# Performance work log

Hardware: AMD Instinct MI355X
Metric: run time of the kernel (lower is better)

Reference implementation:

```python
import jax, jax.numpy as jnp
import numpy as np


def setup_inputs() -> dict:
    key = jax.random.key(0)
    ks = jax.random.split(key, 5)
    B = 8192
    return {
        "x": jax.random.normal(ks[0], (B, 1, 28, 28), dtype=jnp.float32),
        "conv1w": jax.random.normal(ks[1], (3, 196, 1, 2, 2), dtype=jnp.float32),
        "conv2w": jax.random.normal(ks[2], (64, 36, 3, 4, 4), dtype=jnp.float32),
        "fc1w": jax.random.normal(ks[3], (1024, 2304), dtype=jnp.float32),
        "fc2w": jax.random.normal(ks[4], (10, 1024), dtype=jnp.float32),
    }


def reference(x, conv1w, conv2w, fc1w, fc2w):
    # The torch module swaps a fresh filter into conv2d for every output pixel,
    # i.e. an unshared-weight (locally-connected) conv. Each kept pixel is
    # relu(dot(patch, per-pixel filter)), so we unfold patches and contract.
    B = x.shape[0]

    # --- layer 1: 2x2 kernel, stride 2, non-overlapping -> 14x14 = 196 pixels
    # [B,1,28,28] -> [B,14,2,14,2] -> [B,196,4] patches
    p1 = x[:, 0].reshape(B, 14, 2, 14, 2).transpose(0, 1, 3, 2, 4).reshape(B, 196, 4)
    w1 = conv1w.reshape(3, 196, 4)  # [C=3, P=196, K=4]
    out1 = jax.nn.relu(jnp.einsum('bpk,cpk->bcp', p1, w1)).reshape(B, 3, 14, 14)

    # --- layer 2: 4x4 kernel, stride 2 on 14x14 -> 6x6 = 36 pixels, 3 in-ch
    idx = 2 * jnp.arange(6)[:, None] + jnp.arange(4)[None, :]  # [6,4] row/col gather
    t = out1[:, :, idx, :]          # [B,3,6,4,14]
    t = t[:, :, :, :, idx]          # [B,3,6,4,6,4]
    # -> [B, 6, 6, 3, 4, 4] -> [B, 36, 48] (patch features in torch CHW order)
    p2 = t.transpose(0, 2, 4, 1, 3, 5).reshape(B, 36, 48)
    w2 = conv2w.reshape(64, 36, 48)  # [C=64, P=36, K=48]
    out2 = jax.nn.relu(jnp.einsum('bpk,cpk->bcp', p2, w2)).reshape(B, 2304)

    # --- fully connected head (bias-free linears)
    h = jax.nn.relu(out2 @ fc1w.T)   # [B,1024]
    return h @ fc2w.T                # [B,10]
```

## Files before the change

kernel.cpp:

```cpp
#include <hip/hip_runtime.h>
#include <hip/hip_bf16.h>

typedef __attribute__((ext_vector_type(8))) short short8;
typedef __attribute__((ext_vector_type(4))) float f32x4;
typedef __attribute__((ext_vector_type(8))) unsigned short ushort8;
typedef __attribute__((ext_vector_type(4))) unsigned short ushort4v;

__device__ __forceinline__ float bf2f(unsigned short u) {
  union { unsigned int i; float f; } v;
  v.i = ((unsigned int)u) << 16;
  return v.f;
}

__device__ __forceinline__ unsigned short f2bf(float f) {
  union { float f; unsigned int i; } v;
  v.f = f;
  unsigned int x = v.i;
  return (unsigned short)((x + 0x7FFFu + ((x >> 16) & 1u)) >> 16);
}

__device__ __forceinline__ void async_load16(const void* g, void* l) {
  __builtin_amdgcn_global_load_lds(
      (const __attribute__((address_space(1))) unsigned int*)g,
      (__attribute__((address_space(3))) unsigned int*)l, 16, 0, 0);
}

__global__ __launch_bounds__(256) void cvt_permute(
    const float* __restrict__ fc1, unsigned short* __restrict__ out) {
  __shared__ float row[2304];
  const int n = blockIdx.x;
  const float* src = fc1 + (size_t)n * 2304;
  for (int i = threadIdx.x; i < 2304; i += 256) row[i] = src[i];
  __syncthreads();
  unsigned short* dst = out + (size_t)n * 2304;
  for (int i = threadIdx.x; i < 2304; i += 256) {
    int pp = i >> 6, c2 = i & 63;
    dst[i] = f2bf(row[c2 * 36 + pp]);
  }
}

#define LDP 72
__global__ __launch_bounds__(256) void conv_fused3(
    const float* __restrict__ x, const float* __restrict__ w1,
    const float* __restrict__ w2, unsigned short* __restrict__ out2, int B) {
  __shared__ unsigned short s_w2[64 * LDP];
  __shared__ unsigned short s_win[64 * LDP];
  const int tid = threadIdx.x;
  const int b0 = blockIdx.x * 64;
  const int p = blockIdx.y;
  const int u = p / 6, u2 = p % 6;

  {
    const float* w2p = w2 + (size_t)p * 48;
    for (int it = tid; it < 768; it += 256) {
      int c2 = it & 63, q = it >> 6;
      float4 wv = *(const float4*)(w2p + (size_t)c2 * 1728 + 4 * q);
      ushort4v o;
      o[0] = f2bf(wv.x); o[1] = f2bf(wv.y); o[2] = f2bf(wv.z); o[3] = f2bf(wv.w);
      *(ushort4v*)&s_w2[c2 * LDP + 4 * q] = o;
    }
  }

  for (int it = tid; it < 768; it += 256) {
    int bi = it & 63, cv = it >> 6;
    int c = cv >> 2, v = cv & 3;
    int pi = 2 * u + v;
    const float* xb = x + (size_t)(b0 + bi) * 784 + pi * 56 + 4 * u2;
    float4 a0 = *(const float4*)xb;
    float4 a1 = *(const float4*)(xb + 4);
    float4 r0 = *(const float4*)(xb + 28);
    float4 r1 = *(const float4*)(xb + 32);
    const float* wbase = w1 + ((c * 196 + pi * 14 + 2 * u2) << 2);
    float4 q0 = *(const float4*)(wbase);
    float4 q1 = *(const float4*)(wbase + 4);
    float4 q2 = *(const float4*)(wbase + 8);
    float4 q3 = *(const float4*)(wbase + 12);
    ushort4v o;
    o[0] = f2bf(fmaxf(a0.x * q0.x + a0.y * q0.y + r0.x * q0.z + r0.y * q0.w, 0.f));
    o[1] = f2bf(fmaxf(a0.z * q1.x + a0.w * q1.y + r0.z * q1.z + r0.w * q1.w, 0.f));
    o[2] = f2bf(fmaxf(a1.x * q2.x + a1.y * q2.y + r1.x * q2.z + r1.y * q2.w, 0.f));
    o[3] = f2bf(fmaxf(a1.z * q3.x + a1.w * q3.y + r1.z * q3.z + r1.w * q3.w, 0.f));
    *(ushort4v*)&s_win[bi * LDP + 4 * cv] = o;
  }

  {
    int bi = tid >> 2, q = tid & 3;
    ushort4v z = {0, 0, 0, 0};
    *(ushort4v*)&s_win[bi * LDP + 48 + 4 * q] = z;
    *(ushort4v*)&s_w2[bi * LDP + 48 + 4 * q] = z;
  }
  __syncthreads();

  const int lane = tid & 63, wave = tid >> 6;
  const int wm = wave >> 1, wn = wave & 1;
  const int fr = lane & 15, fo = (lane >> 4) * 8;
  f32x4 acc[2][2] = {};
  #pragma unroll
  for (int k2 = 0; k2 < 2; ++k2) {
    short8 af[2], bf[2];
    #pragma unroll
    for (int m = 0; m < 2; ++m)
      af[m] = *(const short8*)&s_win[(wm * 32 + m * 16 + fr) * LDP + k2 * 32 + fo];
    #pragma unroll
    for (int n = 0; n < 2; ++n)
      bf[n] = *(const short8*)&s_w2[(wn * 32 + n * 16 + fr) * LDP + k2 * 32 + fo];
    #pragma unroll
    for (int m = 0; m < 2; ++m)
      #pragma unroll
      for (int n = 0; n < 2; ++n)
        acc[m][n] =
            __builtin_amdgcn_mfma_f32_16x16x32_bf16(af[m], bf[n], acc[m][n], 0, 0, 0);
  }
  __syncthreads();

  unsigned short* s_out = s_win;
  const int r0 = wm * 32 + (lane >> 4) * 4;
  const int c0 = wn * 32 + fr;
  #pragma unroll
  for (int m = 0; m < 2; ++m)
    #pragma unroll
    for (int n = 0; n < 2; ++n)
      #pragma unroll
      for (int j = 0; j < 4; ++j)
        s_out[(r0 + m * 16 + j) * 64 + (c0 + n * 16)] =
            f2bf(fmaxf(acc[m][n][j], 0.f));
  __syncthreads();

  for (int it = tid; it < 512; it += 256) {
    int row = it >> 3, ch = it & 7;
    *(short8*)(out2 + (size_t)(b0 + row) * 2304 + p * 64 + ch * 8) =
        *(const short8*)&s_out[row * 64 + ch * 8];
  }
}

#define GBM 128
#define GBN 128
#define GBK 64

__global__ __launch_bounds__(512) void gemm_fc1_fc2(
    const unsigned short* __restrict__ A,
    const unsigned short* __restrict__ Bw,
    const float* __restrict__ Wfc2,
    float* __restrict__ out,
    int K, int NT) {
  __shared__ unsigned short sA[2 * GBM * GBK];
  __shared__ unsigned short sB[2 * GBN * GBK];
  __shared__ float sW[10 * GBN];
  const int tid = threadIdx.x;
  const int lane = tid & 63;
  const int wave = tid >> 6;
  const int wm = wave >> 2, wn = wave & 3;
  const size_t m0 = (size_t)blockIdx.x * GBM;
  const size_t n0 = (size_t)blockIdx.y * GBN;

  const int r8 = tid >> 3;
  const int c8 = tid & 7;
  const int ksw = (c8 ^ (r8 & 7)) * 8;
  const unsigned short* Ag = A + (m0 + r8) * (size_t)K + ksw;
  const unsigned short* Bg = Bw + (n0 + r8) * (size_t)K + ksw;
  unsigned short* sAp = &sA[r8 * GBK + c8 * 8];
  unsigned short* sBp = &sB[r8 * GBK + c8 * 8];

#define STAGE_A(buf, t, i) \
  async_load16(Ag + (size_t)(t) * GBK + (size_t)(i) * 64 * K, \
               sAp + (buf) * (GBM * GBK) + (i) * 64 * GBK)
#define STAGE_B(buf, t, i) \
  async_load16(Bg + (size_t)(t) * GBK + (size_t)(i) * 64 * K, \
               sBp + (buf) * (GBN * GBK) + (i) * 64 * GBK)
#define STAGE_TILE(buf, t) \
  STAGE_A(buf, t, 0); STAGE_A(buf, t, 1); STAGE_B(buf, t, 0); STAGE_B(buf, t, 1)

  STAGE_TILE(0, 0);

  const int fr = lane & 15, fg = lane >> 4, fx = lane & 7;
  int aBase[4], bBase[2];
  #pragma unroll
  for (int m = 0; m < 4; ++m) aBase[m] = (wm * 64 + m * 16 + fr) * GBK;
  #pragma unroll
  for (int n = 0; n < 2; ++n) bBase[n] = (wn * 32 + n * 16 + fr) * GBK;
  const int jc0 = (fg ^ fx) * 8;
  const int jc1 = jc0 ^ 32;

  f32x4 acc[4][2] = {};

  for (int t = 0; t < NT; ++t) {
    const int cur = t & 1;
    if (t + 1 < NT) {
      STAGE_TILE(cur ^ 1, t + 1);
      asm volatile("s_waitcnt vmcnt(4)" ::: "memory");
    } else {
      asm volatile("s_waitcnt vmcnt(0)" ::: "memory");
    }
    __builtin_amdgcn_s_barrier();

    const unsigned short* As = &sA[cur * GBM * GBK];
    const unsigned short* Bs = &sB[cur * GBN * GBK];
    short8 a0[4], a1[4], b0[2], b1[2];
    #pragma unroll
    for (int m = 0; m < 4; ++m) {
      a0[m] = *(const short8*)&As[aBase[m] + jc0];
      a1[m] = *(const short8*)&As[aBase[m] + jc1];
    }
    #pragma unroll
    for (int n = 0; n < 2; ++n) {
      b0[n] = *(const short8*)&Bs[bBase[n] + jc0];
      b1[n] = *(const short8*)&Bs[bBase[n] + jc1];
    }
    __builtin_amdgcn_s_setprio(1);
    #pragma unroll
    for (int m = 0; m < 4; ++m)
      #pragma unroll
      for (int n = 0; n < 2; ++n)
        acc[m][n] = __builtin_amdgcn_mfma_f32_16x16x32_bf16(a0[m], b0[n],
                                                            acc[m][n], 0, 0, 0);
    #pragma unroll
    for (int m = 0; m < 4; ++m)
      #pragma unroll
      for (int n = 0; n < 2; ++n)
        acc[m][n] = __builtin_amdgcn_mfma_f32_16x16x32_bf16(a1[m], b1[n],
                                                            acc[m][n], 0, 0, 0);
    __builtin_amdgcn_s_setprio(0);
    __builtin_amdgcn_s_barrier();
  }

  for (int i = tid; i < 10 * GBN; i += 512)
    sW[i] = Wfc2[(i >> 7) * 1024 + n0 + (i & 127)];

  unsigned short* hs = sA;
  #pragma unroll
  for (int m = 0; m < 4; ++m)
    #pragma unroll
    for (int n = 0; n < 2; ++n)
      #pragma unroll
      for (int j = 0; j < 4; ++j) {
        int row = wm * 64 + m * 16 + fg * 4 + j;
        int col = wn * 32 + n * 16 + fr;
        hs[row * 128 + (col ^ ((row & 7) << 3))] =
            f2bf(fmaxf(acc[m][n][j], 0.f));
      }
  __syncthreads();

  {
    const int row = tid >> 2;
    const int quar = tid & 3;
    const int r7s = (row & 7) << 3;
    float hv[32];
    #pragma unroll
    for (int c = 0; c < 4; ++c) {
      int base = quar * 32 + c * 8;
      short8 u = *(const short8*)&hs[row * 128 + (base ^ r7s)];
      #pragma unroll
      for (int q = 0; q < 8; ++q) hv[c * 8 + q] = bf2f((unsigned short)u[q]);
    }
    float* op = out + (m0 + row) * 10;
    #pragma unroll
    for (int o = 0; o < 10; ++o) {
      const float* wr = &sW[o * 128 + quar * 32];
      float a = 0.f;
      #pragma unroll
      for (int q = 0; q < 32; ++q) a += hv[q] * wr[q];
      a += __shfl_down(a, 1);
      a += __shfl_down(a, 2);
      if (quar == 0) atomicAdd(&op[o], a);
    }
  }
#undef STAGE_A
#undef STAGE_B
#undef STAGE_TILE
}

extern "C" void kernel_launch(void* const* d_in, const int* in_sizes, int n_in,
                              void* d_out, int out_size, void* d_ws, size_t ws_size,
                              hipStream_t stream) {
  const float* x   = (const float*)d_in[0];
  const float* w1  = (const float*)d_in[1];
  const float* w2  = (const float*)d_in[2];
  const float* fc1 = (const float*)d_in[3];
  const float* fc2 = (const float*)d_in[4];
  float* out = (float*)d_out;
  const int B = in_sizes[0] / 784;

  unsigned short* out2 = (unsigned short*)d_ws;
  unsigned short* fc1b = out2 + (size_t)B * 2304;

  hipMemsetAsync(out, 0, (size_t)out_size * sizeof(float), stream);
  cvt_permute<<<1024, 256, 0, stream>>>(fc1, fc1b);
  dim3 cg(B / 64, 36);
  conv_fused3<<<cg, 256, 0, stream>>>(x, w1, w2, out2, B);
  dim3 g(B / GBM, 1024 / GBN);
  gemm_fc1_fc2<<<g, 512, 0, stream>>>(out2, fc1b, fc2, out, 2304, 2304 / GBK);
}
```

Measured before the change: 102.6 us.

## Restructure fc1 GEMM to 256 threads with 64x64 warp tiles and BK=32

The fc1+fc2 GEMM moves from 512 threads (8 waves, 64x32 per wave) to 256 threads (4 waves, 64x64 per wave) and halves the K tile to 32. It uses a single combined shared buffer with a new swizzle, and the fused fc2 epilogue now splits each row between 2 threads instead of 4. The goal is more register reuse per wave and, with launch_bounds(256,4) and less LDS, more resident blocks per CU. The cost is twice as many K iterations and barriers, more accumulator registers, and a shallower pipeline per stage.

Measured after the change: 111.6 us. 8.8% more time.

```diff
diff --git a/kernel.cpp b/kernel.cpp
--- a/kernel.cpp
+++ b/kernel.cpp
@@ -135,31 +135,32 @@
 
 #define GBM 128
 #define GBN 128
-#define GBK 64
-
-__global__ __launch_bounds__(512) void gemm_fc1_fc2(
+#define GBK 32
+
+__global__ __launch_bounds__(256, 4) void gemm_fc1_fc2(
     const unsigned short* __restrict__ A,
     const unsigned short* __restrict__ Bw,
     const float* __restrict__ Wfc2,
     float* __restrict__ out,
     int K, int NT) {
-  __shared__ unsigned short sA[2 * GBM * GBK];
-  __shared__ unsigned short sB[2 * GBN * GBK];
+  __shared__ unsigned short smem[2 * (GBM + GBN) * GBK];
   __shared__ float sW[10 * GBN];
+  unsigned short* sA = smem;
+  unsigned short* sB = smem + 2 * GBM * GBK;
   const int tid = threadIdx.x;
   const int lane = tid & 63;
   const int wave = tid >> 6;
-  const int wm = wave >> 2, wn = wave & 3;
+  const int wm = wave >> 1, wn = wave & 1;
   const size_t m0 = (size_t)blockIdx.x * GBM;
   const size_t n0 = (size_t)blockIdx.y * GBN;
 
-  const int r8 = tid >> 3;
-  const int c8 = tid & 7;
-  const int ksw = (c8 ^ (r8 & 7)) * 8;
-  const unsigned short* Ag = A + (m0 + r8) * (size_t)K + ksw;
-  const unsigned short* Bg = Bw + (n0 + r8) * (size_t)K + ksw;
-  unsigned short* sAp = &sA[r8 * GBK + c8 * 8];
-  unsigned short* sBp = &sB[r8 * GBK + c8 * 8];
+  const int r4 = tid >> 2;
+  const int c4 = tid & 3;
+  const int ksw = (c4 ^ ((r4 >> 1) & 3)) * 8;
+  const unsigned short* Ag = A + (m0 + r4) * (size_t)K + ksw;
+  const unsigned short* Bg = Bw + (n0 + r4) * (size_t)K + ksw;
+  unsigned short* sAp = &sA[r4 * GBK + c4 * 8];
+  unsigned short* sBp = &sB[r4 * GBK + c4 * 8];
 
 #define STAGE_A(buf, t, i) \
   async_load16(Ag + (size_t)(t) * GBK + (size_t)(i) * 64 * K, \
@@ -172,16 +173,15 @@
 
   STAGE_TILE(0, 0);
 
-  const int fr = lane & 15, fg = lane >> 4, fx = lane & 7;
-  int aBase[4], bBase[2];
-  #pragma unroll
-  for (int m = 0; m < 4; ++m) aBase[m] = (wm * 64 + m * 16 + fr) * GBK;
-  #pragma unroll
-  for (int n = 0; n < 2; ++n) bBase[n] = (wn * 32 + n * 16 + fr) * GBK;
-  const int jc0 = (fg ^ fx) * 8;
-  const int jc1 = jc0 ^ 32;
-
-  f32x4 acc[4][2] = {};
+  const int fr = lane & 15, fg = lane >> 4;
+  const int jc = (fg ^ ((fr >> 1) & 3)) * 8;
+  int aBase[4], bBase[4];
+  #pragma unroll
+  for (int m = 0; m < 4; ++m) aBase[m] = (wm * 64 + m * 16 + fr) * GBK + jc;
+  #pragma unroll
+  for (int n = 0; n < 4; ++n) bBase[n] = (wn * 64 + n * 16 + fr) * GBK + jc;
+
+  f32x4 acc[4][4] = {};
 
   for (int t = 0; t < NT; ++t) {
     const int cur = t & 1;
@@ -195,59 +195,47 @@
 
     const unsigned short* As = &sA[cur * GBM * GBK];
     const unsigned short* Bs = &sB[cur * GBN * GBK];
-    short8 a0[4], a1[4], b0[2], b1[2];
-    #pragma unroll
-    for (int m = 0; m < 4; ++m) {
-      a0[m] = *(const short8*)&As[aBase[m] + jc0];
-      a1[m] = *(const short8*)&As[aBase[m] + jc1];
-    }
-    #pragma unroll
-    for (int n = 0; n < 2; ++n) {
-      b0[n] = *(const short8*)&Bs[bBase[n] + jc0];
-      b1[n] = *(const short8*)&Bs[bBase[n] + jc1];
-    }
+    short8 af[4], bf[4];
+    #pragma unroll
+    for (int m = 0; m < 4; ++m) af[m] = *(const short8*)&As[aBase[m]];
+    #pragma unroll
+    for (int n = 0; n < 4; ++n) bf[n] = *(const short8*)&Bs[bBase[n]];
     __builtin_amdgcn_s_setprio(1);
     #pragma unroll
     for (int m = 0; m < 4; ++m)
       #pragma unroll
-      for (int n = 0; n < 2; ++n)
-        acc[m][n] = __builtin_amdgcn_mfma_f32_16x16x32_bf16(a0[m], b0[n],
-                                                            acc[m][n], 0, 0, 0);
-    #pragma unroll
-    for (int m = 0; m < 4; ++m)
-      #pragma unroll
-      for (int n = 0; n < 2; ++n)
-        acc[m][n] = __builtin_amdgcn_mfma_f32_16x16x32_bf16(a1[m], b1[n],
+      for (int n = 0; n < 4; ++n)
+        acc[m][n] = __builtin_amdgcn_mfma_f32_16x16x32_bf16(af[m], bf[n],
                                                             acc[m][n], 0, 0, 0);
     __builtin_amdgcn_s_setprio(0);
     __builtin_amdgcn_s_barrier();
   }
 
-  for (int i = tid; i < 10 * GBN; i += 512)
+  for (int i = tid; i < 10 * GBN; i += 256)
     sW[i] = Wfc2[(i >> 7) * 1024 + n0 + (i & 127)];
 
-  unsigned short* hs = sA;
+  unsigned short* hs = smem;
   #pragma unroll
   for (int m = 0; m < 4; ++m)
     #pragma unroll
-    for (int n = 0; n < 2; ++n)
+    for (int n = 0; n < 4; ++n)
       #pragma unroll
       for (int j = 0; j < 4; ++j) {
         int row = wm * 64 + m * 16 + fg * 4 + j;
-        int col = wn * 32 + n * 16 + fr;
+        int col = wn * 64 + n * 16 + fr;
         hs[row * 128 + (col ^ ((row & 7) << 3))] =
             f2bf(fmaxf(acc[m][n][j], 0.f));
       }
   __syncthreads();
 
   {
-    const int row = tid >> 2;
-    const int quar = tid & 3;
+    const int row = tid >> 1;
+    const int half = tid & 1;
     const int r7s = (row & 7) << 3;
-    float hv[32];
-    #pragma unroll
-    for (int c = 0; c < 4; ++c) {
-      int base = quar * 32 + c * 8;
+    float hv[64];
+    #pragma unroll
+    for (int c = 0; c < 8; ++c) {
+      int base = half * 64 + c * 8;
       short8 u = *(const short8*)&hs[row * 128 + (base ^ r7s)];
       #pragma unroll
       for (int q = 0; q < 8; ++q) hv[c * 8 + q] = bf2f((unsigned short)u[q]);
@@ -255,13 +243,12 @@
     float* op = out + (m0 + row) * 10;
     #pragma unroll
     for (int o = 0; o < 10; ++o) {
-      const float* wr = &sW[o * 128 + quar * 32];
+      const float* wr = &sW[o * 128 + half * 64];
       float a = 0.f;
       #pragma unroll
-      for (int q = 0; q < 32; ++q) a += hv[q] * wr[q];
+      for (int q = 0; q < 64; ++q) a += hv[q] * wr[q];
       a += __shfl_down(a, 1);
-      a += __shfl_down(a, 2);
-      if (quar == 0) atomicAdd(&op[o], a);
+      if (half == 0) atomicAdd(&op[o], a);
     }
   }
 #undef STAGE_A
@@ -288,5 +275,5 @@
   dim3 cg(B / 64, 36);
   conv_fused3<<<cg, 256, 0, stream>>>(x, w1, w2, out2, B);
   dim3 g(B / GBM, 1024 / GBN);
-  gemm_fc1_fc2<<<g, 512, 0, stream>>>(out2, fc1b, fc2, out, 2304, 2304 / GBK);
-}
+  gemm_fc1_fc2<<<g, 256, 0, stream>>>(out2, fc1b, fc2, out, 2304, 2304 / GBK);
+}
```

## Fold fc1 conversion into conv kernel and split GEMM K-step into two phases

Applied to the files above, without the earlier changes.

Removes the separate cvt_permute launch by adding an extra blockIdx.y slice to the conv kernel, where blocks convert and permute eight fc1 rows each to bf16. This saves a kernel launch and lets the conversion run alongside the conv work. In the GEMM main loop, the B-tile prefetch is moved after the first half of the LDS reads, and each K-tile is split into two read-then-MFMA phases separated by a barrier, so global loads interleave better with compute. The cost is an extra barrier per iteration and tighter waitcnt control. The conversion blocks also process rows serially with two syncs per row, which could leave them as stragglers.

Result: slower. 114.3 us (+11.4%).

```diff
diff --git a/kernel.cpp b/kernel.cpp
--- a/kernel.cpp
+++ b/kernel.cpp
@@ -25,29 +25,34 @@
       (__attribute__((address_space(3))) unsigned int*)l, 16, 0, 0);
 }
 
-__global__ __launch_bounds__(256) void cvt_permute(
-    const float* __restrict__ fc1, unsigned short* __restrict__ out) {
-  __shared__ float row[2304];
-  const int n = blockIdx.x;
-  const float* src = fc1 + (size_t)n * 2304;
-  for (int i = threadIdx.x; i < 2304; i += 256) row[i] = src[i];
-  __syncthreads();
-  unsigned short* dst = out + (size_t)n * 2304;
-  for (int i = threadIdx.x; i < 2304; i += 256) {
-    int pp = i >> 6, c2 = i & 63;
-    dst[i] = f2bf(row[c2 * 36 + pp]);
-  }
-}
-
 #define LDP 72
-__global__ __launch_bounds__(256) void conv_fused3(
+__global__ __launch_bounds__(256) void conv_fused4(
     const float* __restrict__ x, const float* __restrict__ w1,
-    const float* __restrict__ w2, unsigned short* __restrict__ out2, int B) {
+    const float* __restrict__ w2, unsigned short* __restrict__ out2,
+    const float* __restrict__ fc1, unsigned short* __restrict__ fc1b, int B) {
   __shared__ unsigned short s_w2[64 * LDP];
   __shared__ unsigned short s_win[64 * LDP];
   const int tid = threadIdx.x;
+  const int p = blockIdx.y;
+
+  if (p == 36) {
+    float* rowbuf = (float*)s_w2;
+    const int n0 = blockIdx.x * 8;
+    for (int r = 0; r < 8; ++r) {
+      const float* src = fc1 + (size_t)(n0 + r) * 2304;
+      for (int i = tid; i < 2304; i += 256) rowbuf[i] = src[i];
+      __syncthreads();
+      unsigned short* dst = fc1b + (size_t)(n0 + r) * 2304;
+      for (int i = tid; i < 2304; i += 256) {
+        int pp = i >> 6, c2 = i & 63;
+        dst[i] = f2bf(rowbuf[c2 * 36 + pp]);
+      }
+      __syncthreads();
+    }
+    return;
+  }
+
   const int b0 = blockIdx.x * 64;
-  const int p = blockIdx.y;
   const int u = p / 6, u2 = p % 6;
 
   {
@@ -167,10 +172,8 @@
 #define STAGE_B(buf, t, i) \
   async_load16(Bg + (size_t)(t) * GBK + (size_t)(i) * 64 * K, \
                sBp + (buf) * (GBN * GBK) + (i) * 64 * GBK)
-#define STAGE_TILE(buf, t) \
-  STAGE_A(buf, t, 0); STAGE_A(buf, t, 1); STAGE_B(buf, t, 0); STAGE_B(buf, t, 1)
-
-  STAGE_TILE(0, 0);
+
+  STAGE_A(0, 0, 0); STAGE_A(0, 0, 1); STAGE_B(0, 0, 0); STAGE_B(0, 0, 1);
 
   const int fr = lane & 15, fg = lane >> 4, fx = lane & 7;
   int aBase[4], bBase[2];
@@ -185,27 +188,25 @@
 
   for (int t = 0; t < NT; ++t) {
     const int cur = t & 1;
-    if (t + 1 < NT) {
-      STAGE_TILE(cur ^ 1, t + 1);
-      asm volatile("s_waitcnt vmcnt(4)" ::: "memory");
+    const unsigned short* As = &sA[cur * GBM * GBK];
+    const unsigned short* Bs = &sB[cur * GBN * GBK];
+    const bool pf = (t + 1 < NT);
+    if (pf) {
+      STAGE_A(cur ^ 1, t + 1, 0); STAGE_A(cur ^ 1, t + 1, 1);
+      asm volatile("s_waitcnt vmcnt(2)" ::: "memory");
     } else {
       asm volatile("s_waitcnt vmcnt(0)" ::: "memory");
     }
     __builtin_amdgcn_s_barrier();
 
-    const unsigned short* As = &sA[cur * GBM * GBK];
-    const unsigned short* Bs = &sB[cur * GBN * GBK];
-    short8 a0[4], a1[4], b0[2], b1[2];
-    #pragma unroll
-    for (int m = 0; m < 4; ++m) {
-      a0[m] = *(const short8*)&As[aBase[m] + jc0];
-      a1[m] = *(const short8*)&As[aBase[m] + jc1];
-    }
-    #pragma unroll
-    for (int n = 0; n < 2; ++n) {
-      b0[n] = *(const short8*)&Bs[bBase[n] + jc0];
-      b1[n] = *(const short8*)&Bs[bBase[n] + jc1];
-    }
+    short8 a0[4], b0[2];
+    #pragma unroll
+    for (int m = 0; m < 4; ++m) a0[m] = *(const short8*)&As[aBase[m] + jc0];
+    #pragma unroll
+    for (int n = 0; n < 2; ++n) b0[n] = *(const short8*)&Bs[bBase[n] + jc0];
+    if (pf) { STAGE_B(cur ^ 1, t + 1, 0); STAGE_B(cur ^ 1, t + 1, 1); }
+    asm volatile("s_waitcnt lgkmcnt(0)" ::: "memory");
+    __builtin_amdgcn_sched_barrier(0);
     __builtin_amdgcn_s_setprio(1);
     #pragma unroll
     for (int m = 0; m < 4; ++m)
@@ -213,6 +214,17 @@
       for (int n = 0; n < 2; ++n)
         acc[m][n] = __builtin_amdgcn_mfma_f32_16x16x32_bf16(a0[m], b0[n],
                                                             acc[m][n], 0, 0, 0);
+    __builtin_amdgcn_s_setprio(0);
+    __builtin_amdgcn_s_barrier();
+
+    short8 a1[4], b1[2];
+    #pragma unroll
+    for (int m = 0; m < 4; ++m) a1[m] = *(const short8*)&As[aBase[m] + jc1];
+    #pragma unroll
+    for (int n = 0; n < 2; ++n) b1[n] = *(const short8*)&Bs[bBase[n] + jc1];
+    asm volatile("s_waitcnt lgkmcnt(0)" ::: "memory");
+    __builtin_amdgcn_sched_barrier(0);
+    __builtin_amdgcn_s_setprio(1);
     #pragma unroll
     for (int m = 0; m < 4; ++m)
       #pragma unroll
@@ -266,7 +278,6 @@
   }
 #undef STAGE_A
 #undef STAGE_B
-#undef STAGE_TILE
 }
 
 extern "C" void kernel_launch(void* const* d_in, const int* in_sizes, int n_in,
@@ -284,9 +295,8 @@
   unsigned short* fc1b = out2 + (size_t)B * 2304;
 
   hipMemsetAsync(out, 0, (size_t)out_size * sizeof(float), stream);
-  cvt_permute<<<1024, 256, 0, stream>>>(fc1, fc1b);
-  dim3 cg(B / 64, 36);
-  conv_fused3<<<cg, 256, 0, stream>>>(x, w1, w2, out2, B);
+  dim3 cg(B / 64, 37);
+  conv_fused4<<<cg, 256, 0, stream>>>(x, w1, w2, out2, fc1, fc1b, B);
   dim3 g(B / GBM, 1024 / GBN);
   gemm_fc1_fc2<<<g, 512, 0, stream>>>(out2, fc1b, fc2, out, 2304, 2304 / GBK);
 }
```
